# Kernel tuning notes

Hardware: AMD Instinct MI355X
Metric: run time of the kernel (lower is better)

Reference implementation:

```python
import jax, jax.numpy as jnp
import numpy as np

B, NC, C, H, L = 256, 99, 128, 512, 3
N = NC + 1              # nodes per graph (depot + customers)
NT = B * N              # total nodes
EPS = 1e-5


def _edge_index():
    # PyG-style: torch.combinations(arange(n), r=2) -> directed upper-tri edges, replicated per batch
    r, c = np.triu_indices(N, k=1)
    offs = (np.arange(B) * N)[:, None]
    row = (r[None, :] + offs).ravel()
    col = (c[None, :] + offs).ravel()
    # gcn_norm adds self loops
    sl = np.arange(NT)
    row = np.concatenate([row, sl])
    col = np.concatenate([col, sl])
    return jnp.asarray(row, jnp.int32), jnp.asarray(col, jnp.int32)


def _bn(x, g, b):
    # BatchNorm1d in training mode over flattened (B*n, C); biased variance
    m = x.mean(0)
    v = jnp.mean((x - m) ** 2, axis=0)
    return g * (x - m) * jax.lax.rsqrt(v + EPS) + b


def setup_inputs() -> dict:
    key = jax.random.key(0)
    ks = jax.random.split(key, 16)
    f = jax.random.normal
    return dict(
        depot_xy=jax.random.uniform(ks[0], (B, 2), jnp.float32),
        customer_xy=jax.random.uniform(ks[1], (B, NC, 2), jnp.float32),
        demand=jax.random.uniform(ks[2], (B, NC), jnp.float32),
        W_depot=f(ks[3], (2, C), jnp.float32) * 0.5,
        b_depot=f(ks[4], (C,), jnp.float32) * 0.1,
        W_init=f(ks[5], (3, C), jnp.float32) * 0.5,
        b_init=f(ks[6], (C,), jnp.float32) * 0.1,
        gcn_W=f(ks[7], (L, C, C), jnp.float32) / np.sqrt(C),
        gcn_b=f(ks[8], (L, C), jnp.float32) * 0.1,
        bn_gamma=jnp.ones((L, C), jnp.float32),
        bn_beta=jnp.zeros((L, C), jnp.float32),
        ff_W1=f(ks[9], (L, C, H), jnp.float32) / np.sqrt(C),
        ff_b1=f(ks[10], (L, H), jnp.float32) * 0.1,
        ff_W2=f(ks[11], (L, H, C), jnp.float32) / np.sqrt(H),
        ff_b2=f(ks[12], (L, C), jnp.float32) * 0.1,
    )


def reference(depot_xy, customer_xy, demand, W_depot, b_depot, W_init, b_init,
              gcn_W, gcn_b, bn_gamma, bn_beta, ff_W1, ff_b1, ff_W2, ff_b2):
    # initial node embeddings
    depot_e = depot_xy @ W_depot + b_depot                      # [B, C]
    cust_in = jnp.concatenate([customer_xy, demand[..., None]], -1)  # [B, NC, 3]
    cust_e = cust_in @ W_init + b_init                          # [B, NC, C]
    x = jnp.concatenate([depot_e[:, None, :], cust_e], 1).reshape(NT, C)

    row, col = _edge_index()
    # GCN symmetric normalization (with self loops, directed src->dst)
    deg = jax.ops.segment_sum(jnp.ones_like(col, x.dtype), col, num_segments=NT)
    dis = jnp.where(deg > 0, jax.lax.rsqrt(deg), 0.0)
    norm = dis[row] * dis[col]                                  # [E]

    for l in range(L):
        h = x @ gcn_W[l]                                        # [NT, C]
        msg = norm[:, None] * h[row]                            # gather + scale
        agg = jax.ops.segment_sum(msg, col, num_segments=NT) + gcn_b[l]
        x = _bn(x + agg, bn_gamma[l], bn_beta[l])
        ff = jax.nn.relu(x @ ff_W1[l] + ff_b1[l]) @ ff_W2[l] + ff_b2[l]
        x = _bn(x + ff, bn_gamma[l], bn_beta[l])

    nodes = x.reshape(B, N, C)
    return nodes, jnp.mean(nodes, axis=1)
```

## Files before the change

kernel.cpp:

```cpp
#include <hip/hip_runtime.h>

constexpr int kB = 256;
constexpr int kNC = 99;
constexpr int kN = 100;
constexpr int kC = 128;
constexpr int kH = 512;
constexpr int kL = 3;
constexpr int kNT = kB * kN;
constexpr int kRT = 64;
constexpr int kFFBlocks = kNT / kRT;
constexpr float kEps = 1e-5f;

typedef unsigned short u16;
typedef unsigned int u32;
typedef __attribute__((ext_vector_type(8))) __bf16 bf16x8;
typedef __attribute__((ext_vector_type(4))) float f32x4;
typedef __attribute__((ext_vector_type(8))) unsigned short u16x8;

__device__ __forceinline__ u16 f2bf(float x) {
  __bf16 h = (__bf16)x;
  return __builtin_bit_cast(u16, h);
}
__device__ __forceinline__ float bf2f(u16 h) {
  union { u32 u; float f; } v; v.u = ((u32)h) << 16;
  return v.f;
}

__device__ __forceinline__ void affine_from_stats(
    const float* __restrict__ stats, const float* __restrict__ gamma,
    const float* __restrict__ beta, int c, float& sc, float& sh) {
  if (stats != nullptr) {
    float s = stats[c], sq = stats[kC + c];
    float m = s * (1.0f / kNT);
    float v = sq * (1.0f / kNT) - m * m;
    float rs = rsqrtf(v + kEps);
    sc = gamma[c] * rs;
    sh = beta[c] - m * sc;
  } else {
    sc = 1.0f;
    sh = 0.0f;
  }
}

__device__ __forceinline__ void pack_group(
    int g, const float* __restrict__ gcnW, const float* __restrict__ W1,
    const float* __restrict__ W2, u16* __restrict__ wpack) {
  int layer = g / 36864, r = g % 36864;
  const float* src; int shf; u16* base; int isW2 = 0;
  if (r < 4096) {
    src = gcnW + (size_t)layer * kC * kC; shf = 7;
    base = wpack + (size_t)(layer * 288 + 0) * 512;
  } else if (r < 20480) {
    src = W1 + (size_t)layer * kC * kH; shf = 9;
    base = wpack + (size_t)(layer * 288 + 32) * 512; r -= 4096;
  } else {
    src = W2 + (size_t)layer * kH * kC; shf = 7;
    base = wpack + (size_t)(layer * 288 + 160) * 512; r -= 20480; isW2 = 1;
  }
  int e4 = r * 4;
  int k = e4 >> shf, n0 = e4 & ((1 << shf) - 1);
  float4 v = *(const float4*)(src + ((size_t)k << shf) + n0);
  float vv[4] = {v.x, v.y, v.z, v.w};
  int kb = k >> 5, hi = (k >> 3) & 3, j = k & 7;
#pragma unroll
  for (int t = 0; t < 4; ++t) {
    int n = n0 + t;
    int nb = n >> 4, l = hi * 16 + (n & 15);
    int f = isW2 ? (nb * 16 + kb) : (nb * 4 + kb);
    base[(size_t)f * 512 + l * 8 + j] = f2bf(vv[t]);
  }
}

template <bool FIRST>
__global__ __launch_bounds__(256, 4) void k_gcn(
    const u16* __restrict__ yprev, const float* __restrict__ stats_prev,
    const float* __restrict__ gamma_p, const float* __restrict__ beta_p,
    const u16* __restrict__ Wgp, const float* __restrict__ gb,
    float* __restrict__ stats_out, u16* __restrict__ yA,
    const float* __restrict__ dxy, const float* __restrict__ cxy,
    const float* __restrict__ dem, const float* __restrict__ Wd,
    const float* __restrict__ bd, const float* __restrict__ Wi,
    const float* __restrict__ bi, const float* __restrict__ gcnW,
    const float* __restrict__ W1, const float* __restrict__ W2,
    u16* __restrict__ wpack) {
  __shared__ float s_scale[kC], s_shift[kC];
  __shared__ __align__(16) u16 ubuf[112 * 136];
  __shared__ float sP[4][64], s_sum[64], s_sq[64];
  __shared__ float scoord[kN][4];
  __shared__ float swt[7][kC];
  u16 (*xs)[136] = (u16(*)[136])ubuf;
  float* hs = (float*)ubuf;
  const int tid = threadIdx.x;
  const int b = blockIdx.x >> 1, half = blockIdx.x & 1;
  const int wave = tid >> 6, lane = tid & 63;
  const int arow = lane & 15, kofs = (lane >> 4) * 8;
  const int crow = (lane >> 4) * 4, ccol = lane & 15;
  const int nbW = half * 4 + wave;
  bf16x8 bfr[4];
  if (FIRST) {
#pragma unroll
    for (int kb = 0; kb < 4; ++kb)
#pragma unroll
      for (int e = 0; e < 8; ++e) {
        int krow = kb * 32 + (lane >> 4) * 8 + e;
        bfr[kb][e] = (__bf16)gcnW[(size_t)krow * kC + nbW * 16 + (lane & 15)];
      }
  } else {
#pragma unroll
    for (int kb = 0; kb < 4; ++kb)
      bfr[kb] = *(const bf16x8*)(Wgp + (size_t)(nbW * 4 + kb) * 512 + lane * 8);
  }
  if (FIRST) {
    int g = blockIdx.x * 256 + tid;
    if (g < kL * 36864) pack_group(g, gcnW, W1, W2, wpack);
    if (tid < kN) {
      if (tid == 0) {
        scoord[0][0] = dxy[b * 2];
        scoord[0][1] = dxy[b * 2 + 1];
        scoord[0][2] = 0.0f;
      } else {
        int q = b * kNC + tid - 1;
        scoord[tid][0] = cxy[q * 2];
        scoord[tid][1] = cxy[q * 2 + 1];
        scoord[tid][2] = dem[q];
      }
    }
    if (tid < 224) {
      int f = tid * 4, r = f >> 7, c = f & 127;
      const float* s;
      switch (r) {
        case 0: s = Wd + c; break;
        case 1: s = Wd + kC + c; break;
        case 2: s = bd + c; break;
        case 3: s = Wi + c; break;
        case 4: s = Wi + kC + c; break;
        case 5: s = Wi + 2 * kC + c; break;
        default: s = bi + c; break;
      }
      *(float4*)&swt[r][c] = *(const float4*)s;
    }
  }
  if (tid < kC) affine_from_stats(stats_prev, gamma_p, beta_p, tid,
                                  s_scale[tid], s_shift[tid]);
  if (tid < 64) { s_sum[tid] = 0.0f; s_sq[tid] = 0.0f; }
  __syncthreads();
  const size_t gbase = (size_t)b * kN * kC;
#pragma unroll
  for (int i = 0; i < 7; ++i) {
    int li = i * 256 + tid;
    int lr = li >> 4, lc8 = (li & 15) * 8;
    u16x8 o = {0, 0, 0, 0, 0, 0, 0, 0};
    if (lr < kN) {
      if (FIRST) {
        float sx = scoord[lr][0], sy = scoord[lr][1], sd = scoord[lr][2];
#pragma unroll
        for (int e = 0; e < 8; ++e) {
          int c = lc8 + e;
          float g = (lr == 0)
              ? fmaf(sx, swt[0][c], fmaf(sy, swt[1][c], swt[2][c]))
              : fmaf(sx, swt[3][c], fmaf(sy, swt[4][c], fmaf(sd, swt[5][c], swt[6][c])));
          o[e] = f2bf(fmaf(g, s_scale[c], s_shift[c]));
        }
      } else {
        u16x8 hv = *(const u16x8*)(yprev + gbase + (size_t)lr * kC + lc8);
#pragma unroll
        for (int e = 0; e < 8; ++e)
          o[e] = f2bf(fmaf(bf2f(hv[e]), s_scale[lc8 + e], s_shift[lc8 + e]));
      }
    }
    *(u16x8*)&xs[lr][lc8] = o;
  }
  __syncthreads();
  f32x4 acc[7];
#pragma unroll
  for (int t = 0; t < 7; ++t) {
    acc[t] = {0.f, 0.f, 0.f, 0.f};
#pragma unroll
    for (int kb = 0; kb < 4; ++kb) {
      bf16x8 a = *(const bf16x8*)&xs[t * 16 + arow][kb * 32 + kofs];
      acc[t] = __builtin_amdgcn_mfma_f32_16x16x32_bf16(a, bfr[kb], acc[t], 0, 0, 0);
    }
  }
  __syncthreads();
#pragma unroll
  for (int t = 0; t < 7; ++t) {
    int rbase = t * 16 + crow;
#pragma unroll
    for (int r = 0; r < 4; ++r)
      if (rbase + r < kN) hs[(rbase + r) * 68 + wave * 16 + ccol] = acc[t][r];
  }
  __syncthreads();
  const int c = tid & 63, jh = tid >> 6;
  const int ch = half * 64 + c;
  const float sc = s_scale[ch], sh = s_shift[ch];
  const float gbc = gb[ch];
  const int j0 = jh * 25;
  float p = 0.0f;
#pragma unroll
  for (int jj = 0; jj < 25; ++jj)
    p = fmaf(hs[(j0 + jj) * 68 + c], rsqrtf((float)(j0 + jj + 1)), p);
  sP[jh][c] = p;
  __syncthreads();
  float s = 0.0f;
  for (int q = 0; q < jh; ++q) s += sP[q][c];
  float wv0 = 0.f, wv1 = 0.f, wv2 = 0.f, wv3 = 0.f, wd0 = 0.f, wd1 = 0.f, wd2 = 0.f;
  if (FIRST) {
    wv0 = swt[3][ch]; wv1 = swt[4][ch]; wv2 = swt[5][ch]; wv3 = swt[6][ch];
    wd0 = swt[0][ch]; wd1 = swt[1][ch]; wd2 = swt[2][ch];
  }
  float lsum = 0.0f, lsq = 0.0f;
#pragma unroll
  for (int jj = 0; jj < 25; ++jj) {
    int j = j0 + jj;
    float r = rsqrtf((float)(j + 1));
    s = fmaf(hs[j * 68 + c], r, s);
    float xv;
    if (FIRST) {
      float sx = scoord[j][0], sy = scoord[j][1], sd = scoord[j][2];
      xv = (j == 0) ? fmaf(sx, wd0, fmaf(sy, wd1, wd2))
                    : fmaf(sx, wv0, fmaf(sy, wv1, fmaf(sd, wv2, wv3)));
    } else {
      xv = fmaf(bf2f(yprev[gbase + (size_t)j * kC + ch]), sc, sh);
    }
    float yv = xv + fmaf(s, r, gbc);
    yA[gbase + (size_t)j * kC + ch] = f2bf(yv);
    lsum += yv;
    lsq = fmaf(yv, yv, lsq);
  }
  atomicAdd(&s_sum[c], lsum);
  atomicAdd(&s_sq[c], lsq);
  __syncthreads();
  if (tid < 64) {
    atomicAdd(&stats_out[half * 64 + tid], s_sum[tid]);
    atomicAdd(&stats_out[kC + half * 64 + tid], s_sq[tid]);
  }
}

template <bool LAST>
__global__ __launch_bounds__(512, 4) void k_ff(
    const u16* __restrict__ yA, const float* __restrict__ stats_in,
    const float* __restrict__ gamma, const float* __restrict__ beta,
    const u16* __restrict__ W1p, const float* __restrict__ b1,
    const u16* __restrict__ W2p, const float* __restrict__ b2,
    float* __restrict__ stats_out, u16* __restrict__ yB16,
    float* __restrict__ yB32) {
  __shared__ float s_scale[kC], s_shift[kC], s_sum[kC], s_sq[kC];
  __shared__ float s_b1[kH];
  __shared__ u16 xs[kRT][136];
  __shared__ u16 hid[kRT][272];
  const int tid = threadIdx.x;
  const int wave = tid >> 6, lane = tid & 63;
  const int arow = lane & 15, kofs = (lane >> 4) * 8;
  const int crow = (lane >> 4) * 4, ccol = lane & 15;
  if (tid < kC) {
    affine_from_stats(stats_in, gamma, beta, tid, s_scale[tid], s_shift[tid]);
    s_sum[tid] = 0.0f;
    s_sq[tid] = 0.0f;
  }
  if (tid < 128) ((float4*)s_b1)[tid] = ((const float4*)b1)[tid];
  __syncthreads();
  const int rb = blockIdx.x * kRT;
#pragma unroll
  for (int i = 0; i < 2; ++i) {
    int li = i * 512 + tid;
    int lr = li >> 4, lc8 = (li & 15) * 8;
    u16x8 hv = *(const u16x8*)(yA + (size_t)(rb + lr) * kC + lc8);
    u16x8 o;
#pragma unroll
    for (int e = 0; e < 8; ++e)
      o[e] = f2bf(fmaf(bf2f(hv[e]), s_scale[lc8 + e], s_shift[lc8 + e]));
    *(u16x8*)&xs[lr][lc8] = o;
  }
  const int c = wave * 16 + ccol;
  u16 resid[16];
#pragma unroll
  for (int rt = 0; rt < 4; ++rt)
#pragma unroll
    for (int r = 0; r < 4; ++r)
      resid[rt * 4 + r] = yA[(size_t)(rb + rt * 16 + crow + r) * kC + c];
  __syncthreads();

  f32x4 oacc[4] = {{0.f, 0.f, 0.f, 0.f}, {0.f, 0.f, 0.f, 0.f},
                   {0.f, 0.f, 0.f, 0.f}, {0.f, 0.f, 0.f, 0.f}};
  for (int chk = 0; chk < 2; ++chk) {
    bf16x8 bw[8];
#pragma unroll
    for (int kk = 0; kk < 8; ++kk)
      bw[kk] = *(const bf16x8*)(W2p + (size_t)(wave * 16 + chk * 8 + kk) * 512 + lane * 8);
#pragma unroll
    for (int q = 0; q < 2; ++q) {
      const int nb = chk * 16 + wave * 2 + q;
      bf16x8 b1f[4];
#pragma unroll
      for (int kb = 0; kb < 4; ++kb)
        b1f[kb] = *(const bf16x8*)(W1p + (size_t)(nb * 4 + kb) * 512 + lane * 8);
      const int cl = (wave * 2 + q) * 16 + ccol;
      const float bbias = s_b1[chk * 256 + cl];
#pragma unroll
      for (int rt = 0; rt < 4; ++rt) {
        f32x4 acc = {0.f, 0.f, 0.f, 0.f};
#pragma unroll
        for (int kb = 0; kb < 4; ++kb) {
          bf16x8 a = *(const bf16x8*)&xs[rt * 16 + arow][kb * 32 + kofs];
          acc = __builtin_amdgcn_mfma_f32_16x16x32_bf16(a, b1f[kb], acc, 0, 0, 0);
        }
#pragma unroll
        for (int r = 0; r < 4; ++r)
          hid[rt * 16 + crow + r][cl] = f2bf(fmaxf(acc[r] + bbias, 0.0f));
      }
    }
    __syncthreads();
#pragma unroll
    for (int kk = 0; kk < 8; ++kk) {
#pragma unroll
      for (int rt = 0; rt < 4; ++rt) {
        bf16x8 ha = *(const bf16x8*)&hid[rt * 16 + arow][kk * 32 + kofs];
        oacc[rt] = __builtin_amdgcn_mfma_f32_16x16x32_bf16(ha, bw[kk], oacc[rt], 0, 0, 0);
      }
    }
    __syncthreads();
  }

  const float sc = s_scale[c], sh = s_shift[c], bb = b2[c];
  float psum = 0.0f, psq = 0.0f;
#pragma unroll
  for (int rt = 0; rt < 4; ++rt) {
#pragma unroll
    for (int r = 0; r < 4; ++r) {
      int lrow = rt * 16 + crow + r;
      float xv = fmaf(bf2f(resid[rt * 4 + r]), sc, sh);
      float o = oacc[rt][r] + bb + xv;
      if (LAST)
        yB32[(size_t)(rb + lrow) * kC + c] = o;
      else
        yB16[(size_t)(rb + lrow) * kC + c] = f2bf(o);
      psum += o;
      psq = fmaf(o, o, psq);
    }
  }
  atomicAdd(&s_sum[c], psum);
  atomicAdd(&s_sq[c], psq);
  __syncthreads();
  if (tid < kC) {
    atomicAdd(&stats_out[tid], s_sum[tid]);
    atomicAdd(&stats_out[kC + tid], s_sq[tid]);
  }
}

__global__ __launch_bounds__(1024) void k_out(
    const float* __restrict__ yB, const float* __restrict__ stats,
    const float* __restrict__ gamma, const float* __restrict__ beta,
    float* __restrict__ out) {
  __shared__ float sP[8][kC];
  const int b = blockIdx.x;
  const int c = threadIdx.x & 127, jh = threadIdx.x >> 7;
  float sc, sh;
  affine_from_stats(stats, gamma, beta, c, sc, sh);
  const int j0 = (jh < 4) ? jh * 13 : 52 + (jh - 4) * 12;
  const int jc = (jh < 4) ? 13 : 12;
  float acc = 0.0f;
  const size_t base = (size_t)b * kN * kC + c;
  for (int jj = 0; jj < jc; ++jj) {
    int j = j0 + jj;
    float xv = fmaf(yB[base + (size_t)j * kC], sc, sh);
    out[base + (size_t)j * kC] = xv;
    acc += xv;
  }
  sP[jh][c] = acc;
  __syncthreads();
  if (jh == 0) {
    float m = 0.0f;
#pragma unroll
    for (int q = 0; q < 8; ++q) m += sP[q][c];
    out[(size_t)kNT * kC + (size_t)b * kC + c] = m * (1.0f / kN);
  }
}

extern "C" void kernel_launch(void* const* d_in, const int* in_sizes, int n_in,
                              void* d_out, int out_size, void* d_ws, size_t ws_size,
                              hipStream_t stream) {
  const float* depot_xy    = (const float*)d_in[0];
  const float* customer_xy = (const float*)d_in[1];
  const float* demand      = (const float*)d_in[2];
  const float* W_depot     = (const float*)d_in[3];
  const float* b_depot     = (const float*)d_in[4];
  const float* W_init      = (const float*)d_in[5];
  const float* b_init      = (const float*)d_in[6];
  const float* gcn_W       = (const float*)d_in[7];
  const float* gcn_b       = (const float*)d_in[8];
  const float* bn_gamma    = (const float*)d_in[9];
  const float* bn_beta     = (const float*)d_in[10];
  const float* ff_W1       = (const float*)d_in[11];
  const float* ff_b1       = (const float*)d_in[12];
  const float* ff_W2       = (const float*)d_in[13];
  const float* ff_b2       = (const float*)d_in[14];

  u16*   yA16  = (u16*)d_ws;
  u16*   yB16  = yA16 + (size_t)kNT * kC;
  float* yB32  = (float*)(yB16 + (size_t)kNT * kC);
  float* stats = yB32 + (size_t)kNT * kC;
  u16*   wpack = (u16*)(stats + kL * 2 * 2 * kC);

  hipMemsetAsync(stats, 0, kL * 2 * 2 * kC * sizeof(float), stream);
  for (int l = 0; l < kL; ++l) {
    const float* sp = (l == 0) ? nullptr : stats + ((l - 1) * 2 + 1) * 2 * kC;
    const float* gp = (l == 0) ? nullptr : bn_gamma + (l - 1) * kC;
    const float* bp = (l == 0) ? nullptr : bn_beta + (l - 1) * kC;
    float* s0 = stats + (l * 2 + 0) * 2 * kC;
    float* s1 = stats + (l * 2 + 1) * 2 * kC;
    const u16* wg  = wpack + (size_t)(l * 288 + 0) * 512;
    const u16* w1p = wpack + (size_t)(l * 288 + 32) * 512;
    const u16* w2p = wpack + (size_t)(l * 288 + 160) * 512;
    if (l == 0) {
      k_gcn<true><<<kB * 2, 256, 0, stream>>>(
          nullptr, sp, gp, bp, nullptr, gcn_b + l * kC, s0, yA16,
          depot_xy, customer_xy, demand, W_depot, b_depot, W_init, b_init,
          gcn_W, ff_W1, ff_W2, wpack);
    } else {
      k_gcn<false><<<kB * 2, 256, 0, stream>>>(
          yB16, sp, gp, bp, wg, gcn_b + l * kC, s0, yA16,
          nullptr, nullptr, nullptr, nullptr, nullptr, nullptr, nullptr,
          nullptr, nullptr, nullptr, nullptr);
    }
    if (l < kL - 1) {
      k_ff<false><<<kFFBlocks, 512, 0, stream>>>(
          yA16, s0, bn_gamma + l * kC, bn_beta + l * kC,
          w1p, ff_b1 + l * kH, w2p, ff_b2 + l * kC, s1, yB16, nullptr);
    } else {
      k_ff<true><<<kFFBlocks, 512, 0, stream>>>(
          yA16, s0, bn_gamma + l * kC, bn_beta + l * kC,
          w1p, ff_b1 + l * kH, w2p, ff_b2 + l * kC, s1, nullptr, yB32);
    }
  }
  k_out<<<kB, 1024, 0, stream>>>(yB32, stats + (2 * 2 + 1) * 2 * kC,
                                 bn_gamma + 2 * kC, bn_beta + 2 * kC, (float*)d_out);
}
```

Measured before the change: 126.8 us.

## Fuse all layers into one persistent cooperative kernel with grid syncs

Replaces the seven separate kernel launches (GCN, FF per layer, plus output) with a single cooperative kernel of 512 blocks of 512 threads that steps through the phases, separated by grid.sync and thread fences. The GCN phase now runs 8 waves per block, splitting row tiles across the extra waves, and the FF phase processes the hidden dimension in four chunks of 128 to fit a shared LDS buffer. The aim is to remove kernel launch gaps and tail effects. In exchange it adds grid-wide barrier cost, and the larger per-block shared memory and registers may lower occupancy. A multi-kernel fallback is kept for when occupancy is too low.

After: 147.6 us. +16.3%, slower.

```diff
diff --git a/kernel.cpp b/kernel.cpp
--- a/kernel.cpp
+++ b/kernel.cpp
@@ -1,4 +1,7 @@
 #include <hip/hip_runtime.h>
+#include <hip/hip_cooperative_groups.h>
+
+namespace cg = cooperative_groups;
 
 constexpr int kB = 256;
 constexpr int kNC = 99;
@@ -9,6 +12,7 @@
 constexpr int kNT = kB * kN;
 constexpr int kRT = 64;
 constexpr int kFFBlocks = kNT / kRT;
+constexpr int kGrid = 512;
 constexpr float kEps = 1e-5f;
 
 typedef unsigned short u16;
@@ -41,6 +45,26 @@
     sh = 0.0f;
   }
 }
+
+struct Params {
+  const float *dxy, *cxy, *dem, *Wd, *bd, *Wi, *bi;
+  const float *gcnW, *W1raw, *W2raw;
+  const float *gcn_b, *bn_gamma, *bn_beta, *ff_b1, *ff_b2;
+  u16* wpack;
+  float* stats;
+  u16* yA16;
+  u16* yB16;
+  float* yB32;
+  float* out;
+};
+
+struct Smem {
+  float s_scale[kC], s_shift[kC], s_sum[kC], s_sq[kC];
+  float s_b1[kH];
+  float sP[512];
+  float scoord[kN][4];
+  float swt[7][kC];
+};
 
 __device__ __forceinline__ void pack_group(
     int g, const float* __restrict__ gcnW, const float* __restrict__ W1,
@@ -71,204 +95,202 @@
   }
 }
 
-template <bool FIRST>
-__global__ __launch_bounds__(256, 4) void k_gcn(
-    const u16* __restrict__ yprev, const float* __restrict__ stats_prev,
-    const float* __restrict__ gamma_p, const float* __restrict__ beta_p,
-    const u16* __restrict__ Wgp, const float* __restrict__ gb,
-    float* __restrict__ stats_out, u16* __restrict__ yA,
-    const float* __restrict__ dxy, const float* __restrict__ cxy,
-    const float* __restrict__ dem, const float* __restrict__ Wd,
-    const float* __restrict__ bd, const float* __restrict__ Wi,
-    const float* __restrict__ bi, const float* __restrict__ gcnW,
-    const float* __restrict__ W1, const float* __restrict__ W2,
-    u16* __restrict__ wpack) {
-  __shared__ float s_scale[kC], s_shift[kC];
-  __shared__ __align__(16) u16 ubuf[112 * 136];
-  __shared__ float sP[4][64], s_sum[64], s_sq[64];
-  __shared__ float scoord[kN][4];
-  __shared__ float swt[7][kC];
-  u16 (*xs)[136] = (u16(*)[136])ubuf;
-  float* hs = (float*)ubuf;
+__device__ __forceinline__ void gcn_phase(const Params& p, int l, int gid,
+                                          u16* ubuf, Smem& sm) {
   const int tid = threadIdx.x;
-  const int b = blockIdx.x >> 1, half = blockIdx.x & 1;
+  const int b = gid >> 1, half = gid & 1;
   const int wave = tid >> 6, lane = tid & 63;
   const int arow = lane & 15, kofs = (lane >> 4) * 8;
   const int crow = (lane >> 4) * 4, ccol = lane & 15;
-  const int nbW = half * 4 + wave;
+  const int nbl = wave & 3, th = wave >> 2;
+  const int nbW = half * 4 + nbl;
+  const float* sp = l ? p.stats + ((l - 1) * 2 + 1) * 2 * kC : nullptr;
+  const float* gp = l ? p.bn_gamma + (l - 1) * kC : nullptr;
+  const float* bp = l ? p.bn_beta + (l - 1) * kC : nullptr;
+  float* s0 = p.stats + (size_t)(l * 2) * 2 * kC;
+  const u16* Wgp = p.wpack + (size_t)(l * 288) * 512;
+  u16 (*xs)[136] = (u16(*)[136])ubuf;
+  float* hs = (float*)ubuf;
+
   bf16x8 bfr[4];
-  if (FIRST) {
+  if (l == 0) {
 #pragma unroll
     for (int kb = 0; kb < 4; ++kb)
 #pragma unroll
       for (int e = 0; e < 8; ++e) {
         int krow = kb * 32 + (lane >> 4) * 8 + e;
-        bfr[kb][e] = (__bf16)gcnW[(size_t)krow * kC + nbW * 16 + (lane & 15)];
-      }
+        bfr[kb][e] = (__bf16)p.gcnW[(size_t)krow * kC + nbW * 16 + (lane & 15)];
+      }
+    int g = gid * 512 + tid;
+    if (g < kL * 36864) pack_group(g, p.gcnW, p.W1raw, p.W2raw, p.wpack);
+    if (tid < kN) {
+      if (tid == 0) {
+        sm.scoord[0][0] = p.dxy[b * 2];
+        sm.scoord[0][1] = p.dxy[b * 2 + 1];
+        sm.scoord[0][2] = 0.0f;
+      } else {
+        int q = b * kNC + tid - 1;
+        sm.scoord[tid][0] = p.cxy[q * 2];
+        sm.scoord[tid][1] = p.cxy[q * 2 + 1];
+        sm.scoord[tid][2] = p.dem[q];
+      }
+    }
+    if (tid >= 256 && tid < 480) {
+      int f = (tid - 256) * 4, r = f >> 7, c = f & 127;
+      const float* s;
+      switch (r) {
+        case 0: s = p.Wd + c; break;
+        case 1: s = p.Wd + kC + c; break;
+        case 2: s = p.bd + c; break;
+        case 3: s = p.Wi + c; break;
+        case 4: s = p.Wi + kC + c; break;
+        case 5: s = p.Wi + 2 * kC + c; break;
+        default: s = p.bi + c; break;
+      }
+      *(float4*)&sm.swt[r][c] = *(const float4*)s;
+    }
   } else {
 #pragma unroll
     for (int kb = 0; kb < 4; ++kb)
       bfr[kb] = *(const bf16x8*)(Wgp + (size_t)(nbW * 4 + kb) * 512 + lane * 8);
   }
-  if (FIRST) {
-    int g = blockIdx.x * 256 + tid;
-    if (g < kL * 36864) pack_group(g, gcnW, W1, W2, wpack);
-    if (tid < kN) {
-      if (tid == 0) {
-        scoord[0][0] = dxy[b * 2];
-        scoord[0][1] = dxy[b * 2 + 1];
-        scoord[0][2] = 0.0f;
-      } else {
-        int q = b * kNC + tid - 1;
-        scoord[tid][0] = cxy[q * 2];
-        scoord[tid][1] = cxy[q * 2 + 1];
-        scoord[tid][2] = dem[q];
-      }
-    }
-    if (tid < 224) {
-      int f = tid * 4, r = f >> 7, c = f & 127;
-      const float* s;
-      switch (r) {
-        case 0: s = Wd + c; break;
-        case 1: s = Wd + kC + c; break;
-        case 2: s = bd + c; break;
-        case 3: s = Wi + c; break;
-        case 4: s = Wi + kC + c; break;
-        case 5: s = Wi + 2 * kC + c; break;
-        default: s = bi + c; break;
-      }
-      *(float4*)&swt[r][c] = *(const float4*)s;
-    }
-  }
-  if (tid < kC) affine_from_stats(stats_prev, gamma_p, beta_p, tid,
-                                  s_scale[tid], s_shift[tid]);
-  if (tid < 64) { s_sum[tid] = 0.0f; s_sq[tid] = 0.0f; }
+  if (tid < kC) affine_from_stats(sp, gp, bp, tid, sm.s_scale[tid], sm.s_shift[tid]);
+  if (tid < 64) { sm.s_sum[tid] = 0.0f; sm.s_sq[tid] = 0.0f; }
   __syncthreads();
   const size_t gbase = (size_t)b * kN * kC;
 #pragma unroll
-  for (int i = 0; i < 7; ++i) {
-    int li = i * 256 + tid;
-    int lr = li >> 4, lc8 = (li & 15) * 8;
-    u16x8 o = {0, 0, 0, 0, 0, 0, 0, 0};
-    if (lr < kN) {
-      if (FIRST) {
-        float sx = scoord[lr][0], sy = scoord[lr][1], sd = scoord[lr][2];
-#pragma unroll
-        for (int e = 0; e < 8; ++e) {
-          int c = lc8 + e;
-          float g = (lr == 0)
-              ? fmaf(sx, swt[0][c], fmaf(sy, swt[1][c], swt[2][c]))
-              : fmaf(sx, swt[3][c], fmaf(sy, swt[4][c], fmaf(sd, swt[5][c], swt[6][c])));
-          o[e] = f2bf(fmaf(g, s_scale[c], s_shift[c]));
+  for (int i = 0; i < 4; ++i) {
+    int li = i * 512 + tid;
+    if (li < 1792) {
+      int lr = li >> 4, lc8 = (li & 15) * 8;
+      u16x8 o = {0, 0, 0, 0, 0, 0, 0, 0};
+      if (lr < kN) {
+        if (l == 0) {
+          float sx = sm.scoord[lr][0], sy = sm.scoord[lr][1], sd = sm.scoord[lr][2];
+#pragma unroll
+          for (int e = 0; e < 8; ++e) {
+            int c = lc8 + e;
+            float g = (lr == 0)
+                ? fmaf(sx, sm.swt[0][c], fmaf(sy, sm.swt[1][c], sm.swt[2][c]))
+                : fmaf(sx, sm.swt[3][c],
+                       fmaf(sy, sm.swt[4][c], fmaf(sd, sm.swt[5][c], sm.swt[6][c])));
+            o[e] = f2bf(fmaf(g, sm.s_scale[c], sm.s_shift[c]));
+          }
+        } else {
+          u16x8 hv = *(const u16x8*)(p.yB16 + gbase + (size_t)lr * kC + lc8);
+#pragma unroll
+          for (int e = 0; e < 8; ++e)
+            o[e] = f2bf(fmaf(bf2f(hv[e]), sm.s_scale[lc8 + e], sm.s_shift[lc8 + e]));
         }
-      } else {
-        u16x8 hv = *(const u16x8*)(yprev + gbase + (size_t)lr * kC + lc8);
-#pragma unroll
-        for (int e = 0; e < 8; ++e)
-          o[e] = f2bf(fmaf(bf2f(hv[e]), s_scale[lc8 + e], s_shift[lc8 + e]));
-      }
-    }
-    *(u16x8*)&xs[lr][lc8] = o;
-  }
-  __syncthreads();
-  f32x4 acc[7];
-#pragma unroll
-  for (int t = 0; t < 7; ++t) {
-    acc[t] = {0.f, 0.f, 0.f, 0.f};
-#pragma unroll
-    for (int kb = 0; kb < 4; ++kb) {
-      bf16x8 a = *(const bf16x8*)&xs[t * 16 + arow][kb * 32 + kofs];
-      acc[t] = __builtin_amdgcn_mfma_f32_16x16x32_bf16(a, bfr[kb], acc[t], 0, 0, 0);
-    }
-  }
-  __syncthreads();
-#pragma unroll
-  for (int t = 0; t < 7; ++t) {
-    int rbase = t * 16 + crow;
-#pragma unroll
-    for (int r = 0; r < 4; ++r)
-      if (rbase + r < kN) hs[(rbase + r) * 68 + wave * 16 + ccol] = acc[t][r];
+      }
+      *(u16x8*)&xs[lr][lc8] = o;
+    }
+  }
+  __syncthreads();
+  f32x4 acc[4];
+  const int t0 = th * 4, tcnt = th ? 3 : 4;
+#pragma unroll
+  for (int tt = 0; tt < 4; ++tt) {
+    acc[tt] = {0.f, 0.f, 0.f, 0.f};
+    if (tt < tcnt) {
+      int t = t0 + tt;
+#pragma unroll
+      for (int kb = 0; kb < 4; ++kb) {
+        bf16x8 a = *(const bf16x8*)&xs[t * 16 + arow][kb * 32 + kofs];
+        acc[tt] = __builtin_amdgcn_mfma_f32_16x16x32_bf16(a, bfr[kb], acc[tt], 0, 0, 0);
+      }
+    }
+  }
+  __syncthreads();
+#pragma unroll
+  for (int tt = 0; tt < 4; ++tt) {
+    if (tt < tcnt) {
+      int rbase = (t0 + tt) * 16 + crow;
+#pragma unroll
+      for (int r = 0; r < 4; ++r)
+        if (rbase + r < kN) hs[(rbase + r) * 68 + nbl * 16 + ccol] = acc[tt][r];
+    }
   }
   __syncthreads();
   const int c = tid & 63, jh = tid >> 6;
   const int ch = half * 64 + c;
-  const float sc = s_scale[ch], sh = s_shift[ch];
-  const float gbc = gb[ch];
-  const int j0 = jh * 25;
-  float p = 0.0f;
-#pragma unroll
-  for (int jj = 0; jj < 25; ++jj)
-    p = fmaf(hs[(j0 + jj) * 68 + c], rsqrtf((float)(j0 + jj + 1)), p);
-  sP[jh][c] = p;
+  const float sc = sm.s_scale[ch], sh = sm.s_shift[ch];
+  const float gbc = p.gcn_b[l * kC + ch];
+  const int j0 = (jh < 4) ? jh * 13 : 52 + (jh - 4) * 12;
+  const int jcnt = (jh < 4) ? 13 : 12;
+  float pp = 0.0f;
+  for (int jj = 0; jj < jcnt; ++jj) {
+    int j = j0 + jj;
+    pp = fmaf(hs[j * 68 + c], rsqrtf((float)(j + 1)), pp);
+  }
+  sm.sP[jh * 64 + c] = pp;
   __syncthreads();
   float s = 0.0f;
-  for (int q = 0; q < jh; ++q) s += sP[q][c];
-  float wv0 = 0.f, wv1 = 0.f, wv2 = 0.f, wv3 = 0.f, wd0 = 0.f, wd1 = 0.f, wd2 = 0.f;
-  if (FIRST) {
-    wv0 = swt[3][ch]; wv1 = swt[4][ch]; wv2 = swt[5][ch]; wv3 = swt[6][ch];
-    wd0 = swt[0][ch]; wd1 = swt[1][ch]; wd2 = swt[2][ch];
+  for (int q = 0; q < jh; ++q) s += sm.sP[q * 64 + c];
+  float wv0 = 0.f, wv1 = 0.f, wv2 = 0.f, wv3 = 0.f;
+  float wd0 = 0.f, wd1 = 0.f, wd2 = 0.f;
+  if (l == 0) {
+    wv0 = sm.swt[3][ch]; wv1 = sm.swt[4][ch]; wv2 = sm.swt[5][ch]; wv3 = sm.swt[6][ch];
+    wd0 = sm.swt[0][ch]; wd1 = sm.swt[1][ch]; wd2 = sm.swt[2][ch];
   }
   float lsum = 0.0f, lsq = 0.0f;
-#pragma unroll
-  for (int jj = 0; jj < 25; ++jj) {
+  for (int jj = 0; jj < jcnt; ++jj) {
     int j = j0 + jj;
     float r = rsqrtf((float)(j + 1));
     s = fmaf(hs[j * 68 + c], r, s);
     float xv;
-    if (FIRST) {
-      float sx = scoord[j][0], sy = scoord[j][1], sd = scoord[j][2];
+    if (l == 0) {
+      float sx = sm.scoord[j][0], sy = sm.scoord[j][1], sd = sm.scoord[j][2];
       xv = (j == 0) ? fmaf(sx, wd0, fmaf(sy, wd1, wd2))
                     : fmaf(sx, wv0, fmaf(sy, wv1, fmaf(sd, wv2, wv3)));
     } else {
-      xv = fmaf(bf2f(yprev[gbase + (size_t)j * kC + ch]), sc, sh);
+      xv = fmaf(bf2f(p.yB16[gbase + (size_t)j * kC + ch]), sc, sh);
     }
     float yv = xv + fmaf(s, r, gbc);
-    yA[gbase + (size_t)j * kC + ch] = f2bf(yv);
+    p.yA16[gbase + (size_t)j * kC + ch] = f2bf(yv);
     lsum += yv;
     lsq = fmaf(yv, yv, lsq);
   }
-  atomicAdd(&s_sum[c], lsum);
-  atomicAdd(&s_sq[c], lsq);
+  atomicAdd(&sm.s_sum[c], lsum);
+  atomicAdd(&sm.s_sq[c], lsq);
   __syncthreads();
   if (tid < 64) {
-    atomicAdd(&stats_out[half * 64 + tid], s_sum[tid]);
-    atomicAdd(&stats_out[kC + half * 64 + tid], s_sq[tid]);
-  }
-}
-
-template <bool LAST>
-__global__ __launch_bounds__(512, 4) void k_ff(
-    const u16* __restrict__ yA, const float* __restrict__ stats_in,
-    const float* __restrict__ gamma, const float* __restrict__ beta,
-    const u16* __restrict__ W1p, const float* __restrict__ b1,
-    const u16* __restrict__ W2p, const float* __restrict__ b2,
-    float* __restrict__ stats_out, u16* __restrict__ yB16,
-    float* __restrict__ yB32) {
-  __shared__ float s_scale[kC], s_shift[kC], s_sum[kC], s_sq[kC];
-  __shared__ float s_b1[kH];
-  __shared__ u16 xs[kRT][136];
-  __shared__ u16 hid[kRT][272];
+    atomicAdd(&s0[half * 64 + tid], sm.s_sum[tid]);
+    atomicAdd(&s0[kC + half * 64 + tid], sm.s_sq[tid]);
+  }
+}
+
+__device__ __forceinline__ void ff_phase(const Params& p, int l, int gid,
+                                         u16* ubuf, Smem& sm) {
+  const bool last = (l == kL - 1);
   const int tid = threadIdx.x;
   const int wave = tid >> 6, lane = tid & 63;
   const int arow = lane & 15, kofs = (lane >> 4) * 8;
   const int crow = (lane >> 4) * 4, ccol = lane & 15;
+  const float* s0 = p.stats + (size_t)(l * 2) * 2 * kC;
+  float* s1 = p.stats + (size_t)(l * 2 + 1) * 2 * kC;
+  const u16* W1p = p.wpack + (size_t)(l * 288 + 32) * 512;
+  const u16* W2p = p.wpack + (size_t)(l * 288 + 160) * 512;
+  u16 (*xs)[136] = (u16(*)[136])ubuf;
+  u16 (*hid)[136] = (u16(*)[136])(ubuf + 8704);
   if (tid < kC) {
-    affine_from_stats(stats_in, gamma, beta, tid, s_scale[tid], s_shift[tid]);
-    s_sum[tid] = 0.0f;
-    s_sq[tid] = 0.0f;
-  }
-  if (tid < 128) ((float4*)s_b1)[tid] = ((const float4*)b1)[tid];
-  __syncthreads();
-  const int rb = blockIdx.x * kRT;
+    affine_from_stats(s0, p.bn_gamma + l * kC, p.bn_beta + l * kC, tid,
+                      sm.s_scale[tid], sm.s_shift[tid]);
+    sm.s_sum[tid] = 0.0f;
+    sm.s_sq[tid] = 0.0f;
+  }
+  if (tid < 128) ((float4*)sm.s_b1)[tid] = ((const float4*)(p.ff_b1 + l * kH))[tid];
+  __syncthreads();
+  const int rb = gid * kRT;
 #pragma unroll
   for (int i = 0; i < 2; ++i) {
     int li = i * 512 + tid;
     int lr = li >> 4, lc8 = (li & 15) * 8;
-    u16x8 hv = *(const u16x8*)(yA + (size_t)(rb + lr) * kC + lc8);
+    u16x8 hv = *(const u16x8*)(p.yA16 + (size_t)(rb + lr) * kC + lc8);
     u16x8 o;
 #pragma unroll
     for (int e = 0; e < 8; ++e)
-      o[e] = f2bf(fmaf(bf2f(hv[e]), s_scale[lc8 + e], s_shift[lc8 + e]));
+      o[e] = f2bf(fmaf(bf2f(hv[e]), sm.s_scale[lc8 + e], sm.s_shift[lc8 + e]));
     *(u16x8*)&xs[lr][lc8] = o;
   }
   const int c = wave * 16 + ccol;
@@ -277,51 +299,47 @@
   for (int rt = 0; rt < 4; ++rt)
 #pragma unroll
     for (int r = 0; r < 4; ++r)
-      resid[rt * 4 + r] = yA[(size_t)(rb + rt * 16 + crow + r) * kC + c];
+      resid[rt * 4 + r] = p.yA16[(size_t)(rb + rt * 16 + crow + r) * kC + c];
   __syncthreads();
 
   f32x4 oacc[4] = {{0.f, 0.f, 0.f, 0.f}, {0.f, 0.f, 0.f, 0.f},
                    {0.f, 0.f, 0.f, 0.f}, {0.f, 0.f, 0.f, 0.f}};
-  for (int chk = 0; chk < 2; ++chk) {
-    bf16x8 bw[8];
-#pragma unroll
-    for (int kk = 0; kk < 8; ++kk)
-      bw[kk] = *(const bf16x8*)(W2p + (size_t)(wave * 16 + chk * 8 + kk) * 512 + lane * 8);
-#pragma unroll
-    for (int q = 0; q < 2; ++q) {
-      const int nb = chk * 16 + wave * 2 + q;
-      bf16x8 b1f[4];
-#pragma unroll
-      for (int kb = 0; kb < 4; ++kb)
-        b1f[kb] = *(const bf16x8*)(W1p + (size_t)(nb * 4 + kb) * 512 + lane * 8);
-      const int cl = (wave * 2 + q) * 16 + ccol;
-      const float bbias = s_b1[chk * 256 + cl];
+  for (int chk = 0; chk < 4; ++chk) {
+    bf16x8 bw[4];
+#pragma unroll
+    for (int kb = 0; kb < 4; ++kb)
+      bw[kb] = *(const bf16x8*)(W2p + (size_t)(wave * 16 + chk * 4 + kb) * 512 + lane * 8);
+    const int nb = chk * 8 + wave;
+    bf16x8 b1f[4];
+#pragma unroll
+    for (int kb = 0; kb < 4; ++kb)
+      b1f[kb] = *(const bf16x8*)(W1p + (size_t)(nb * 4 + kb) * 512 + lane * 8);
+    const float bbias = sm.s_b1[chk * 128 + c];
+#pragma unroll
+    for (int rt = 0; rt < 4; ++rt) {
+      f32x4 acc = {0.f, 0.f, 0.f, 0.f};
+#pragma unroll
+      for (int kb = 0; kb < 4; ++kb) {
+        bf16x8 a = *(const bf16x8*)&xs[rt * 16 + arow][kb * 32 + kofs];
+        acc = __builtin_amdgcn_mfma_f32_16x16x32_bf16(a, b1f[kb], acc, 0, 0, 0);
+      }
+#pragma unroll
+      for (int r = 0; r < 4; ++r)
+        hid[rt * 16 + crow + r][c] = f2bf(fmaxf(acc[r] + bbias, 0.0f));
+    }
+    __syncthreads();
+#pragma unroll
+    for (int kb = 0; kb < 4; ++kb) {
 #pragma unroll
       for (int rt = 0; rt < 4; ++rt) {
-        f32x4 acc = {0.f, 0.f, 0.f, 0.f};
-#pragma unroll
-        for (int kb = 0; kb < 4; ++kb) {
-          bf16x8 a = *(const bf16x8*)&xs[rt * 16 + arow][kb * 32 + kofs];
-          acc = __builtin_amdgcn_mfma_f32_16x16x32_bf16(a, b1f[kb], acc, 0, 0, 0);
-        }
-#pragma unroll
-        for (int r = 0; r < 4; ++r)
-          hid[rt * 16 + crow + r][cl] = f2bf(fmaxf(acc[r] + bbias, 0.0f));
+        bf16x8 ha = *(const bf16x8*)&hid[rt * 16 + arow][kb * 32 + kofs];
+        oacc[rt] = __builtin_amdgcn_mfma_f32_16x16x32_bf16(ha, bw[kb], oacc[rt], 0, 0, 0);
       }
     }
     __syncthreads();
-#pragma unroll
-    for (int kk = 0; kk < 8; ++kk) {
-#pragma unroll
-      for (int rt = 0; rt < 4; ++rt) {
-        bf16x8 ha = *(const bf16x8*)&hid[rt * 16 + arow][kk * 32 + kofs];
-        oacc[rt] = __builtin_amdgcn_mfma_f32_16x16x32_bf16(ha, bw[kk], oacc[rt], 0, 0, 0);
-      }
-    }
-    __syncthreads();
-  }
-
-  const float sc = s_scale[c], sh = s_shift[c], bb = b2[c];
+  }
+  const float sc = sm.s_scale[c], sh = sm.s_shift[c];
+  const float bb = p.ff_b2[l * kC + c];
   float psum = 0.0f, psq = 0.0f;
 #pragma unroll
   for (int rt = 0; rt < 4; ++rt) {
@@ -330,108 +348,127 @@
       int lrow = rt * 16 + crow + r;
       float xv = fmaf(bf2f(resid[rt * 4 + r]), sc, sh);
       float o = oacc[rt][r] + bb + xv;
-      if (LAST)
-        yB32[(size_t)(rb + lrow) * kC + c] = o;
+      if (last)
+        p.yB32[(size_t)(rb + lrow) * kC + c] = o;
       else
-        yB16[(size_t)(rb + lrow) * kC + c] = f2bf(o);
+        p.yB16[(size_t)(rb + lrow) * kC + c] = f2bf(o);
       psum += o;
       psq = fmaf(o, o, psq);
     }
   }
-  atomicAdd(&s_sum[c], psum);
-  atomicAdd(&s_sq[c], psq);
+  atomicAdd(&sm.s_sum[c], psum);
+  atomicAdd(&sm.s_sq[c], psq);
   __syncthreads();
   if (tid < kC) {
-    atomicAdd(&stats_out[tid], s_sum[tid]);
-    atomicAdd(&stats_out[kC + tid], s_sq[tid]);
-  }
-}
-
-__global__ __launch_bounds__(1024) void k_out(
-    const float* __restrict__ yB, const float* __restrict__ stats,
-    const float* __restrict__ gamma, const float* __restrict__ beta,
-    float* __restrict__ out) {
-  __shared__ float sP[8][kC];
-  const int b = blockIdx.x;
-  const int c = threadIdx.x & 127, jh = threadIdx.x >> 7;
-  float sc, sh;
-  affine_from_stats(stats, gamma, beta, c, sc, sh);
-  const int j0 = (jh < 4) ? jh * 13 : 52 + (jh - 4) * 12;
-  const int jc = (jh < 4) ? 13 : 12;
+    atomicAdd(&s1[tid], sm.s_sum[tid]);
+    atomicAdd(&s1[kC + tid], sm.s_sq[tid]);
+  }
+}
+
+__device__ __forceinline__ void out_phase(const Params& p, int gid, Smem& sm) {
+  const int tid = threadIdx.x;
+  const float* sf = p.stats + (size_t)(2 * 2 + 1) * 2 * kC;
+  if (tid < kC)
+    affine_from_stats(sf, p.bn_gamma + 2 * kC, p.bn_beta + 2 * kC, tid,
+                      sm.s_scale[tid], sm.s_shift[tid]);
+  __syncthreads();
+  const int c = tid & 127, jh = tid >> 7;
+  const float sc = sm.s_scale[c], sh = sm.s_shift[c];
   float acc = 0.0f;
-  const size_t base = (size_t)b * kN * kC + c;
-  for (int jj = 0; jj < jc; ++jj) {
-    int j = j0 + jj;
-    float xv = fmaf(yB[base + (size_t)j * kC], sc, sh);
-    out[base + (size_t)j * kC] = xv;
+  const size_t base = (size_t)gid * kN * kC + c;
+  const int j0 = jh * 25;
+#pragma unroll
+  for (int jj = 0; jj < 25; ++jj) {
+    float xv = fmaf(p.yB32[base + (size_t)(j0 + jj) * kC], sc, sh);
+    p.out[base + (size_t)(j0 + jj) * kC] = xv;
     acc += xv;
   }
-  sP[jh][c] = acc;
-  __syncthreads();
-  if (jh == 0) {
-    float m = 0.0f;
-#pragma unroll
-    for (int q = 0; q < 8; ++q) m += sP[q][c];
-    out[(size_t)kNT * kC + (size_t)b * kC + c] = m * (1.0f / kN);
-  }
+  sm.sP[jh * kC + c] = acc;
+  __syncthreads();
+  if (jh == 0)
+    p.out[(size_t)kNT * kC + (size_t)gid * kC + c] =
+        (sm.sP[0 * kC + c] + sm.sP[1 * kC + c] + sm.sP[2 * kC + c] +
+         sm.sP[3 * kC + c]) * (1.0f / kN);
+}
+
+__global__ __launch_bounds__(512, 4) void k_gnn(Params p) {
+  cg::grid_group grid = cg::this_grid();
+  __shared__ __align__(16) u16 ubuf[17408];
+  __shared__ Smem sm;
+  const int gid = blockIdx.x;
+  for (int l = 0; l < kL; ++l) {
+    gcn_phase(p, l, gid, ubuf, sm);
+    __threadfence();
+    grid.sync();
+    __threadfence();
+    if (gid < kFFBlocks) ff_phase(p, l, gid, ubuf, sm);
+    __threadfence();
+    grid.sync();
+    __threadfence();
+  }
+  if (gid < kB) out_phase(p, gid, sm);
+}
+
+__global__ __launch_bounds__(512, 4) void k_gcn_only(Params p, int l) {
+  __shared__ __align__(16) u16 ubuf[17408];
+  __shared__ Smem sm;
+  gcn_phase(p, l, blockIdx.x, ubuf, sm);
+}
+__global__ __launch_bounds__(512, 4) void k_ff_only(Params p, int l) {
+  __shared__ __align__(16) u16 ubuf[17408];
+  __shared__ Smem sm;
+  ff_phase(p, l, blockIdx.x, ubuf, sm);
+}
+__global__ __launch_bounds__(512) void k_out_only(Params p) {
+  __shared__ Smem sm;
+  out_phase(p, blockIdx.x, sm);
 }
 
 extern "C" void kernel_launch(void* const* d_in, const int* in_sizes, int n_in,
                               void* d_out, int out_size, void* d_ws, size_t ws_size,
                               hipStream_t stream) {
-  const float* depot_xy    = (const float*)d_in[0];
-  const float* customer_xy = (const float*)d_in[1];
-  const float* demand      = (const float*)d_in[2];
-  const float* W_depot     = (const float*)d_in[3];
-  const float* b_depot     = (const float*)d_in[4];
-  const float* W_init      = (const float*)d_in[5];
-  const float* b_init      = (const float*)d_in[6];
-  const float* gcn_W       = (const float*)d_in[7];
-  const float* gcn_b       = (const float*)d_in[8];
-  const float* bn_gamma    = (const float*)d_in[9];
-  const float* bn_beta     = (const float*)d_in[10];
-  const float* ff_W1       = (const float*)d_in[11];
-  const float* ff_b1       = (const float*)d_in[12];
-  const float* ff_W2       = (const float*)d_in[13];
-  const float* ff_b2       = (const float*)d_in[14];
-
   u16*   yA16  = (u16*)d_ws;
   u16*   yB16  = yA16 + (size_t)kNT * kC;
   float* yB32  = (float*)(yB16 + (size_t)kNT * kC);
   float* stats = yB32 + (size_t)kNT * kC;
   u16*   wpack = (u16*)(stats + kL * 2 * 2 * kC);
 
+  Params p;
+  p.dxy = (const float*)d_in[0];
+  p.cxy = (const float*)d_in[1];
+  p.dem = (const float*)d_in[2];
+  p.Wd  = (const float*)d_in[3];
+  p.bd  = (const float*)d_in[4];
+  p.Wi  = (const float*)d_in[5];
+  p.bi  = (const float*)d_in[6];
+  p.gcnW = (const float*)d_in[7];
+  p.gcn_b = (const float*)d_in[8];
+  p.bn_gamma = (const float*)d_in[9];
+  p.bn_beta = (const float*)d_in[10];
+  p.W1raw = (const float*)d_in[11];
+  p.ff_b1 = (const float*)d_in[12];
+  p.W2raw = (const float*)d_in[13];
+  p.ff_b2 = (const float*)d_in[14];
+  p.wpack = wpack;
+  p.stats = stats;
+  p.yA16 = yA16;
+  p.yB16 = yB16;
+  p.yB32 = yB32;
+  p.out = (float*)d_out;
+
   hipMemsetAsync(stats, 0, kL * 2 * 2 * kC * sizeof(float), stream);
-  for (int l = 0; l < kL; ++l) {
-    const float* sp = (l == 0) ? nullptr : stats + ((l - 1) * 2 + 1) * 2 * kC;
-    const float* gp = (l == 0) ? nullptr : bn_gamma + (l - 1) * kC;
-    const float* bp = (l == 0) ? nullptr : bn_beta + (l - 1) * kC;
-    float* s0 = stats + (l * 2 + 0) * 2 * kC;
-    float* s1 = stats + (l * 2 + 1) * 2 * kC;
-    const u16* wg  = wpack + (size_t)(l * 288 + 0) * 512;
-    const u16* w1p = wpack + (size_t)(l * 288 + 32) * 512;
-    const u16* w2p = wpack + (size_t)(l * 288 + 160) * 512;
-    if (l == 0) {
-      k_gcn<true><<<kB * 2, 256, 0, stream>>>(
-          nullptr, sp, gp, bp, nullptr, gcn_b + l * kC, s0, yA16,
-          depot_xy, customer_xy, demand, W_depot, b_depot, W_init, b_init,
-          gcn_W, ff_W1, ff_W2, wpack);
-    } else {
-      k_gcn<false><<<kB * 2, 256, 0, stream>>>(
-          yB16, sp, gp, bp, wg, gcn_b + l * kC, s0, yA16,
-          nullptr, nullptr, nullptr, nullptr, nullptr, nullptr, nullptr,
-          nullptr, nullptr, nullptr, nullptr);
-    }
-    if (l < kL - 1) {
-      k_ff<false><<<kFFBlocks, 512, 0, stream>>>(
-          yA16, s0, bn_gamma + l * kC, bn_beta + l * kC,
-          w1p, ff_b1 + l * kH, w2p, ff_b2 + l * kC, s1, yB16, nullptr);
-    } else {
-      k_ff<true><<<kFFBlocks, 512, 0, stream>>>(
-          yA16, s0, bn_gamma + l * kC, bn_beta + l * kC,
-          w1p, ff_b1 + l * kH, w2p, ff_b2 + l * kC, s1, nullptr, yB32);
-    }
-  }
-  k_out<<<kB, 1024, 0, stream>>>(yB32, stats + (2 * 2 + 1) * 2 * kC,
-                                 bn_gamma + 2 * kC, bn_beta + 2 * kC, (float*)d_out);
-}
+
+  int nb = 0;
+  hipError_t oe = hipOccupancyMaxActiveBlocksPerMultiprocessor(&nb, k_gnn, 512, 0);
+  if (oe == hipSuccess && nb >= 2) {
+    void* args[] = {(void*)&p};
+    hipLaunchCooperativeKernel((const void*)k_gnn, dim3(kGrid), dim3(512), args,
+                               0, stream);
+  } else {
+    for (int l = 0; l < kL; ++l) {
+      k_gcn_only<<<kGrid, 512, 0, stream>>>(p, l);
+      k_ff_only<<<kFFBlocks, 512, 0, stream>>>(p, l);
+    }
+    k_out_only<<<kB, 512, 0, stream>>>(p);
+  }
+}
```
